# Performance work log

Measured on AMD Instinct MI355X. Metric: run time of the kernel, lower is better.

Reference implementation:

```python
import jax, jax.numpy as jnp
import numpy as np

N, E, D_IN, HEADS, C = 100000, 1600000, 128, 4, 32  # C = out_channels per head


def setup_inputs() -> dict:
    key = jax.random.key(0)
    ks = jax.random.split(key, 10)
    s = 1.0 / np.sqrt(D_IN)
    return {
        "x": jax.random.normal(ks[0], (N, D_IN), jnp.float32),
        "edge_index": jax.random.randint(ks[1], (2, E), 0, N, jnp.int64),
        "Wq": jax.random.normal(ks[2], (D_IN, HEADS * C), jnp.float32) * s,
        "bq": jnp.zeros((HEADS * C,), jnp.float32),
        "Wk": jax.random.normal(ks[3], (D_IN, HEADS * C), jnp.float32) * s,
        "bk": jnp.zeros((HEADS * C,), jnp.float32),
        "Wv": jax.random.normal(ks[4], (D_IN, HEADS * C), jnp.float32) * s,
        "bv": jnp.zeros((HEADS * C,), jnp.float32),
        "Wskip": jax.random.normal(ks[5], (D_IN, HEADS * C), jnp.float32) * s,
        "bskip": jnp.zeros((HEADS * C,), jnp.float32),
    }


def reference(x, edge_index, Wq, bq, Wk, bk, Wv, bv, Wskip, bskip):
    n = x.shape[0]
    src, dst = edge_index[0], edge_index[1]  # message flows src (j) -> dst (i)
    q = (x @ Wq + bq).reshape(n, HEADS, C)
    k = (x @ Wk + bk).reshape(n, HEADS, C)
    v = (x @ Wv + bv).reshape(n, HEADS, C)

    # per-edge attention logits [E, H]
    alpha = jnp.einsum('ehc,ehc->eh', q[dst], k[src]) / jnp.sqrt(jnp.float32(C))

    # segment softmax over incoming edges of each target node
    m = jax.ops.segment_max(alpha, dst, num_segments=n)          # [N, H]
    p = jnp.exp(alpha - m[dst])                                   # [E, H]
    z = jax.ops.segment_sum(p, dst, num_segments=n)               # [N, H]
    w = p / (z[dst] + 1e-16)                                      # [E, H]

    # softmax-weighted scatter aggregation of values
    out = jax.ops.segment_sum(v[src] * w[:, :, None], dst, num_segments=n)
    out = out.reshape(n, HEADS * C)

    # root/skip connection (beta=False default: plain add)
    out = out + x @ Wskip + bskip
    return out
```

## Files before the change

### kernel.cpp

```cpp
#include <hip/hip_runtime.h>

#define DIN 128
#define NHEADS 4
#define CH 32
#define MT 64
#define NPB 256
#define EPB_IT 25
#define BCAP 6144

#define ST_H 136

typedef _Float16 h8 __attribute__((ext_vector_type(8)));
typedef _Float16 h2 __attribute__((ext_vector_type(2)));
typedef float f4 __attribute__((ext_vector_type(4)));

__global__ __launch_bounds__(256) void prep_w(
    const float* __restrict__ Wq, const float* __restrict__ Wk,
    const float* __restrict__ Wv, const float* __restrict__ Wsk,
    _Float16* __restrict__ wt)
{
    int i = blockIdx.x * 256 + threadIdx.x;
    if (i >= 4 * 16384) return;
    int mat = i >> 14;
    int rem = i & 16383;
    int n  = rem >> 7;
    int kk = rem & 127;
    const float* W = (mat == 0) ? Wq : (mat == 1) ? Wk : (mat == 2) ? Wv : Wsk;
    wt[i] = (_Float16)W[kk * 128 + n];
}

__global__ __launch_bounds__(256) void qkvs_mat(
    const float* __restrict__ x, const _Float16* __restrict__ wt,
    const float* __restrict__ bq, const float* __restrict__ bk,
    const float* __restrict__ bv, const float* __restrict__ bsk,
    _Float16* __restrict__ qh, _Float16* __restrict__ kh,
    _Float16* __restrict__ vh, _Float16* __restrict__ skiph, int N)
{
    __shared__ _Float16 Sbuf[MT * ST_H];
    const int t = threadIdx.x;
    const int mat = blockIdx.x;
    const int rowBase = blockIdx.y * MT;

    for (int i = t; i < MT * 16; i += 256) {
        int r  = i >> 4;
        int c8 = i & 15;
        int gr = rowBase + r;
        _Float16 h[8];
        if (gr < N) {
            float4 f0 = reinterpret_cast<const float4*>(x)[(size_t)gr * 32 + c8 * 2];
            float4 f1 = reinterpret_cast<const float4*>(x)[(size_t)gr * 32 + c8 * 2 + 1];
            h[0] = (_Float16)f0.x; h[1] = (_Float16)f0.y;
            h[2] = (_Float16)f0.z; h[3] = (_Float16)f0.w;
            h[4] = (_Float16)f1.x; h[5] = (_Float16)f1.y;
            h[6] = (_Float16)f1.z; h[7] = (_Float16)f1.w;
        } else {
            #pragma unroll
            for (int j = 0; j < 8; ++j) h[j] = (_Float16)0.f;
        }
        *reinterpret_cast<uint4*>(&Sbuf[r * 128 + ((c8 ^ (r & 7)) << 3)]) =
            *reinterpret_cast<uint4*>(h);
    }
    __syncthreads();

    const int wid  = t >> 6;
    const int l    = t & 63;
    const int lm   = l & 15;
    const int quad = l >> 4;

    const _Float16* __restrict__ Bsrc = wt + (size_t)mat * 16384;

    f4 acc[8];
    #pragma unroll
    for (int nt = 0; nt < 8; ++nt)
        acc[nt] = (f4){0.f, 0.f, 0.f, 0.f};

    #pragma unroll
    for (int kq = 0; kq < 4; ++kq) {
        const int c8 = kq * 4 + quad;
        const int k0 = c8 << 3;
        h8 a0 = *reinterpret_cast<const h8*>(
            &Sbuf[(wid * 16 + lm) * 128 + ((c8 ^ (lm & 7)) << 3)]);
        #pragma unroll
        for (int nt = 0; nt < 8; ++nt) {
            h8 b = *reinterpret_cast<const h8*>(
                &Bsrc[(size_t)(nt * 16 + lm) * 128 + k0]);
            acc[nt] = __builtin_amdgcn_mfma_f32_16x16x32_f16(a0, b, acc[nt], 0, 0, 0);
        }
    }
    __syncthreads();

    const float* bias = (mat == 0) ? bq : (mat == 1) ? bk : (mat == 2) ? bv : bsk;

    #pragma unroll
    for (int nt = 0; nt < 8; ++nt) {
        int col = nt * 16 + lm;
        float bsv = bias[col];
        int row = wid * 16 + quad * 4;
        #pragma unroll
        for (int i2 = 0; i2 < 4; ++i2)
            Sbuf[(row + i2) * ST_H + col] = (_Float16)(acc[nt][i2] + bsv);
    }
    __syncthreads();

    _Float16* __restrict__ dst = (mat == 0) ? qh : (mat == 1) ? kh
                               : (mat == 2) ? vh : skiph;
    for (int j = t; j < MT * 16; j += 256) {
        int r  = j >> 4;
        int c0 = (j & 15) << 3;
        int gr = rowBase + r;
        if (gr < N)
            *reinterpret_cast<uint4*>(&dst[(size_t)gr * 128 + c0]) =
                *reinterpret_cast<const uint4*>(&Sbuf[r * ST_H + c0]);
    }
}

__global__ __launch_bounds__(256) void bucket_scatter(
    const int* __restrict__ ei, int* __restrict__ bcur,
    unsigned* __restrict__ pairs, int E, int nb)
{
    __shared__ int cnt[512];
    int t = threadIdx.x;
    for (int b = t; b < nb; b += 256) cnt[b] = 0;
    __syncthreads();

    long long e0 = (long long)blockIdx.x * (256 * EPB_IT);
    int ps[EPB_IT], pd[EPB_IT];
    #pragma unroll
    for (int j = 0; j < EPB_IT; ++j) {
        long long e = e0 + j * 256 + t;
        if (e < E) {
            ps[j] = ei[e];
            pd[j] = ei[(size_t)E + e];
            atomicAdd(&cnt[pd[j] >> 8], 1);
        } else pd[j] = -1;
    }
    __syncthreads();
    for (int b = t; b < nb; b += 256) {
        int c = cnt[b];
        if (c) cnt[b] = b * BCAP + atomicAdd(&bcur[b], c);
    }
    __syncthreads();
    #pragma unroll
    for (int j = 0; j < EPB_IT; ++j) {
        if (pd[j] >= 0) {
            int pos = atomicAdd(&cnt[pd[j] >> 8], 1);
            pairs[pos] = ((unsigned)ps[j] << 8) | ((unsigned)pd[j] & 255u);
        }
    }
}

__global__ __launch_bounds__(512) void scan_buckets(
    const int* __restrict__ bcur, int* __restrict__ boff, int nb)
{
    __shared__ int ws[8];
    int t = threadIdx.x, lane = t & 63, wid = t >> 6;
    int v = (t < nb) ? bcur[t] : 0;
    int s = v;
    #pragma unroll
    for (int off = 1; off < 64; off <<= 1) {
        int n = __shfl_up(s, off);
        if (lane >= off) s += n;
    }
    if (lane == 63) ws[wid] = s;
    __syncthreads();
    int add = 0;
    for (int w = 0; w < wid; ++w) add += ws[w];
    int excl = s - v + add;
    if (t < nb) boff[t] = excl;
    if (t == nb - 1) boff[nb] = excl + v;
}

__global__ __launch_bounds__(256) void bucket_finalize(
    const unsigned* __restrict__ pairs, const int* __restrict__ bcur,
    const int* __restrict__ boff,
    int* __restrict__ rowptr, int* __restrict__ sorted, int N, int nb)
{
    __shared__ int cnt[NPB];
    __shared__ int cur[NPB];
    __shared__ int ws[4];
    __shared__ int sbuf[BCAP];
    int b = blockIdx.x, t = threadIdx.x;
    cnt[t] = 0;
    __syncthreads();
    size_t r0 = (size_t)b * BCAP;
    int sz = bcur[b];
    int w0 = boff[b];
    for (int i = t; i < sz; i += 256)
        atomicAdd(&cnt[pairs[r0 + i] & (NPB - 1)], 1);
    __syncthreads();

    int v = cnt[t];
    int lane = t & 63, wid = t >> 6;
    int incl = v;
    #pragma unroll
    for (int off = 1; off < 64; off <<= 1) {
        int n = __shfl_up(incl, off);
        if (lane >= off) incl += n;
    }
    if (lane == 63) ws[wid] = incl;
    __syncthreads();
    int add = 0;
    for (int w = 0; w < wid; ++w) add += ws[w];
    int lbase = (incl - v) + add;

    int node = b * NPB + t;
    if (node < N) rowptr[node] = w0 + lbase;
    if (b == nb - 1 && t == 0) rowptr[N] = boff[nb];
    cur[t] = lbase;
    __syncthreads();

    for (int i = t; i < sz; i += 256) {
        unsigned pr = pairs[r0 + i];
        int lpos = atomicAdd(&cur[pr & (NPB - 1)], 1);
        sbuf[lpos] = (int)(pr >> 8);
    }
    __syncthreads();
    for (int i = t; i < sz; i += 256)
        sorted[w0 + i] = sbuf[i];
}

__device__ inline float4 cvt4(unsigned lo, unsigned hi) {
    union { unsigned u[2]; _Float16 h[4]; } c;
    c.u[0] = lo; c.u[1] = hi;
    return make_float4((float)c.h[0], (float)c.h[1], (float)c.h[2], (float)c.h[3]);
}

__device__ inline h2 as_h2(unsigned u) {
    union { unsigned u; h2 h; } c;
    c.u = u;
    return c.h;
}

__global__ __launch_bounds__(256) void node_aggregate(
    const _Float16* __restrict__ q, const _Float16* __restrict__ kh,
    const _Float16* __restrict__ vh, const _Float16* __restrict__ skiph,
    const int* __restrict__ rowptr, const int* __restrict__ srcs,
    float* __restrict__ out, int N)
{
    int gid  = blockIdx.x * 256 + threadIdx.x;
    int node = gid >> 5;
    if (node >= N) return;
    int l = gid & 31;

    uint2 qu = reinterpret_cast<const uint2*>(q + (size_t)node * 128)[l];
    h2 qa = as_h2(qu.x), qb = as_h2(qu.y);

    float4 acc = make_float4(0.f, 0.f, 0.f, 0.f);
    float z = 0.f;

    const uint2* k2 = reinterpret_cast<const uint2*>(kh);
    const uint2* v2 = reinterpret_cast<const uint2*>(vh);
    const float SC = 0.17677669529663687f;
    int e0 = rowptr[node], e1 = rowptr[node + 1];
    int e = e0;

    for (; e + 8 <= e1; e += 8) {
        int s[8];
        #pragma unroll
        for (int j = 0; j < 8; ++j) s[j] = srcs[e + j];
        uint2 kr[8], vr[8];
        #pragma unroll
        for (int j = 0; j < 8; ++j) kr[j] = k2[(size_t)s[j] * 32 + l];
        #pragma unroll
        for (int j = 0; j < 8; ++j) vr[j] = v2[(size_t)s[j] * 32 + l];

        float sv[8];
        #pragma unroll
        for (int j = 0; j < 8; ++j) {
            sv[j] = __builtin_amdgcn_fdot2(qa, as_h2(kr[j].x),
                    __builtin_amdgcn_fdot2(qb, as_h2(kr[j].y), 0.f, false), false);
        }
        #pragma unroll
        for (int j = 0; j < 8; ++j) sv[j] += __shfl_xor(sv[j], 1);
        #pragma unroll
        for (int j = 0; j < 8; ++j) sv[j] += __shfl_xor(sv[j], 2);
        #pragma unroll
        for (int j = 0; j < 8; ++j) sv[j] += __shfl_xor(sv[j], 4);

        #pragma unroll
        for (int j = 0; j < 8; ++j) {
            float p = __expf(sv[j] * SC);
            float4 v = cvt4(vr[j].x, vr[j].y);
            z += p;
            acc.x += p * v.x; acc.y += p * v.y;
            acc.z += p * v.z; acc.w += p * v.w;
        }
    }
    for (; e < e1; ++e) {
        int s0 = srcs[e];
        uint2 kr = k2[(size_t)s0 * 32 + l];
        uint2 vr = v2[(size_t)s0 * 32 + l];
        float sa = __builtin_amdgcn_fdot2(qa, as_h2(kr.x),
                   __builtin_amdgcn_fdot2(qb, as_h2(kr.y), 0.f, false), false);
        sa += __shfl_xor(sa, 1);
        sa += __shfl_xor(sa, 2);
        sa += __shfl_xor(sa, 4);
        float pa = __expf(sa * SC);
        float4 v0 = cvt4(vr.x, vr.y);
        z += pa;
        acc.x += pa * v0.x; acc.y += pa * v0.y;
        acc.z += pa * v0.z; acc.w += pa * v0.w;
    }

    uint2 su = reinterpret_cast<const uint2*>(skiph + (size_t)node * 128)[l];
    float4 sk = cvt4(su.x, su.y);
    float inv = 1.f / (z + 1e-16f);
    float4 o;
    o.x = sk.x + acc.x * inv; o.y = sk.y + acc.y * inv;
    o.z = sk.z + acc.z * inv; o.w = sk.w + acc.w * inv;
    reinterpret_cast<float4*>(out)[(size_t)node * 32 + l] = o;
}

extern "C" void kernel_launch(void* const* d_in, const int* in_sizes, int n_in,
                              void* d_out, int out_size, void* d_ws, size_t ws_size,
                              hipStream_t stream)
{
    const float* x   = (const float*)d_in[0];
    const int*   ei  = (const int*)d_in[1];
    const float* Wq  = (const float*)d_in[2];
    const float* bq  = (const float*)d_in[3];
    const float* Wk  = (const float*)d_in[4];
    const float* bk  = (const float*)d_in[5];
    const float* Wv  = (const float*)d_in[6];
    const float* bv  = (const float*)d_in[7];
    const float* Wsk = (const float*)d_in[8];
    const float* bsk = (const float*)d_in[9];
    float* out = (float*)d_out;

    const int N = in_sizes[0] / DIN;
    const int E = in_sizes[1] / 2;
    const int nb = (N + NPB - 1) / NPB;

    _Float16* qh    = (_Float16*)d_ws;
    _Float16* kh    = qh + (size_t)N * DIN;
    _Float16* vh    = kh + (size_t)N * DIN;
    _Float16* skiph = vh + (size_t)N * DIN;
    _Float16* wt    = skiph + (size_t)N * DIN;
    unsigned* pairs = (unsigned*)(wt + 4 * 16384);
    int* sorted   = (int*)(pairs + (size_t)nb * BCAP);
    int* rowptr   = sorted + E;
    int* bcur     = rowptr + (N + 1);
    int* boff     = bcur + 512;

    hipMemsetAsync(bcur, 0, 512 * sizeof(int), stream);

    prep_w<<<(4 * 16384 + 255) / 256, 256, 0, stream>>>(Wq, Wk, Wv, Wsk, wt);

    dim3 ggrid(4, (N + MT - 1) / MT);
    qkvs_mat<<<ggrid, 256, 0, stream>>>(x, wt, bq, bk, bv, bsk,
                                        qh, kh, vh, skiph, N);

    int sb = (E + 256 * EPB_IT - 1) / (256 * EPB_IT);
    bucket_scatter<<<sb, 256, 0, stream>>>(ei, bcur, pairs, E, nb);
    scan_buckets<<<1, 512, 0, stream>>>(bcur, boff, nb);
    bucket_finalize<<<nb, 256, 0, stream>>>(pairs, bcur, boff, rowptr, sorted, N, nb);

    int ab = (N * 32 + 255) / 256;
    node_aggregate<<<ab, 256, 0, stream>>>(qh, kh, vh, skiph, rowptr, sorted, out, N);
}
```

Before: 389.0 us.

## Interleave K and V per node and compute projection pairs per block

The projection kernel now computes two weight matrices per block (Q+skip, or K+V) and reuses the loaded x tile, halving the number of x reads. K and V are written into one interleaved buffer so that each lane's 4 K halves and 4 V halves sit next to each other. The aggregation kernel can then fetch both with a single 16-byte load per edge instead of two separate 8-byte gathers. This cuts the number of gather transactions in the edge loop, at the cost of more shared memory and registers in the projection kernel.

New measurement: 381.1 us. -2.0%, faster.

```diff
diff --git a/kernel.cpp b/kernel.cpp
--- a/kernel.cpp
+++ b/kernel.cpp
@@ -9,6 +9,7 @@
 #define BCAP 6144
 
 #define ST_H 136
+#define ST_KV 264
 
 typedef _Float16 h8 __attribute__((ext_vector_type(8)));
 typedef _Float16 h2 __attribute__((ext_vector_type(2)));
@@ -29,16 +30,16 @@
     wt[i] = (_Float16)W[kk * 128 + n];
 }
 
-__global__ __launch_bounds__(256) void qkvs_mat(
+__global__ __launch_bounds__(256) void qkvs_pair(
     const float* __restrict__ x, const _Float16* __restrict__ wt,
     const float* __restrict__ bq, const float* __restrict__ bk,
     const float* __restrict__ bv, const float* __restrict__ bsk,
-    _Float16* __restrict__ qh, _Float16* __restrict__ kh,
-    _Float16* __restrict__ vh, _Float16* __restrict__ skiph, int N)
-{
-    __shared__ _Float16 Sbuf[MT * ST_H];
+    _Float16* __restrict__ qh, _Float16* __restrict__ kvh,
+    _Float16* __restrict__ skiph, int N)
+{
+    __shared__ _Float16 Sbuf[17408];
     const int t = threadIdx.x;
-    const int mat = blockIdx.x;
+    const int pair = blockIdx.x;
     const int rowBase = blockIdx.y * MT;
 
     for (int i = t; i < MT * 16; i += 256) {
@@ -67,50 +68,87 @@
     const int lm   = l & 15;
     const int quad = l >> 4;
 
-    const _Float16* __restrict__ Bsrc = wt + (size_t)mat * 16384;
-
-    f4 acc[8];
-    #pragma unroll
-    for (int nt = 0; nt < 8; ++nt)
-        acc[nt] = (f4){0.f, 0.f, 0.f, 0.f};
-
+    h8 afrag[4];
     #pragma unroll
     for (int kq = 0; kq < 4; ++kq) {
-        const int c8 = kq * 4 + quad;
-        const int k0 = c8 << 3;
-        h8 a0 = *reinterpret_cast<const h8*>(
+        int c8 = kq * 4 + quad;
+        afrag[kq] = *reinterpret_cast<const h8*>(
             &Sbuf[(wid * 16 + lm) * 128 + ((c8 ^ (lm & 7)) << 3)]);
-        #pragma unroll
-        for (int nt = 0; nt < 8; ++nt) {
-            h8 b = *reinterpret_cast<const h8*>(
-                &Bsrc[(size_t)(nt * 16 + lm) * 128 + k0]);
-            acc[nt] = __builtin_amdgcn_mfma_f32_16x16x32_f16(a0, b, acc[nt], 0, 0, 0);
-        }
-    }
-    __syncthreads();
-
-    const float* bias = (mat == 0) ? bq : (mat == 1) ? bk : (mat == 2) ? bv : bsk;
-
-    #pragma unroll
-    for (int nt = 0; nt < 8; ++nt) {
-        int col = nt * 16 + lm;
-        float bsv = bias[col];
-        int row = wid * 16 + quad * 4;
-        #pragma unroll
-        for (int i2 = 0; i2 < 4; ++i2)
-            Sbuf[(row + i2) * ST_H + col] = (_Float16)(acc[nt][i2] + bsv);
-    }
-    __syncthreads();
-
-    _Float16* __restrict__ dst = (mat == 0) ? qh : (mat == 1) ? kh
-                               : (mat == 2) ? vh : skiph;
-    for (int j = t; j < MT * 16; j += 256) {
-        int r  = j >> 4;
-        int c0 = (j & 15) << 3;
-        int gr = rowBase + r;
-        if (gr < N)
-            *reinterpret_cast<uint4*>(&dst[(size_t)gr * 128 + c0]) =
-                *reinterpret_cast<const uint4*>(&Sbuf[r * ST_H + c0]);
+    }
+    __syncthreads();
+
+    #pragma unroll
+    for (int half = 0; half < 2; ++half) {
+        const int mat = (pair == 0) ? (half == 0 ? 0 : 3)
+                                    : (half == 0 ? 1 : 2);
+        const _Float16* __restrict__ Bsrc = wt + (size_t)mat * 16384;
+
+        f4 acc[8];
+        #pragma unroll
+        for (int nt = 0; nt < 8; ++nt)
+            acc[nt] = (f4){0.f, 0.f, 0.f, 0.f};
+
+        #pragma unroll
+        for (int kq = 0; kq < 4; ++kq) {
+            const int k0 = (kq * 4 + quad) << 3;
+            #pragma unroll
+            for (int nt = 0; nt < 8; ++nt) {
+                h8 b = *reinterpret_cast<const h8*>(
+                    &Bsrc[(size_t)(nt * 16 + lm) * 128 + k0]);
+                acc[nt] = __builtin_amdgcn_mfma_f32_16x16x32_f16(afrag[kq], b, acc[nt], 0, 0, 0);
+            }
+        }
+
+        const float* bias = (mat == 0) ? bq : (mat == 1) ? bk : (mat == 2) ? bv : bsk;
+
+        if (pair == 0) {
+            _Float16* St = Sbuf + half * (MT * ST_H);
+            #pragma unroll
+            for (int nt = 0; nt < 8; ++nt) {
+                int col = nt * 16 + lm;
+                float bsv = bias[col];
+                int row = wid * 16 + quad * 4;
+                #pragma unroll
+                for (int i2 = 0; i2 < 4; ++i2)
+                    St[(row + i2) * ST_H + col] = (_Float16)(acc[nt][i2] + bsv);
+            }
+        } else {
+            const int off = half * 4;
+            #pragma unroll
+            for (int nt = 0; nt < 8; ++nt) {
+                int col = nt * 16 + lm;
+                float bsv = bias[col];
+                int row = wid * 16 + quad * 4;
+                int sc = ((col >> 2) << 3) + (col & 3) + off;
+                #pragma unroll
+                for (int i2 = 0; i2 < 4; ++i2)
+                    Sbuf[(row + i2) * ST_KV + sc] = (_Float16)(acc[nt][i2] + bsv);
+            }
+        }
+    }
+    __syncthreads();
+
+    if (pair == 0) {
+        for (int j = t; j < 2048; j += 256) {
+            int half = j >> 10;
+            int jj = j & 1023;
+            int r  = jj >> 4;
+            int c0 = (jj & 15) << 3;
+            int gr = rowBase + r;
+            _Float16* __restrict__ dst = half ? skiph : qh;
+            if (gr < N)
+                *reinterpret_cast<uint4*>(&dst[(size_t)gr * 128 + c0]) =
+                    *reinterpret_cast<const uint4*>(&Sbuf[half * (MT * ST_H) + r * ST_H + c0]);
+        }
+    } else {
+        for (int j = t; j < 2048; j += 256) {
+            int r = j >> 5;
+            int g = j & 31;
+            int gr = rowBase + r;
+            if (gr < N)
+                *reinterpret_cast<uint4*>(&kvh[(size_t)gr * 256 + g * 8]) =
+                    *reinterpret_cast<const uint4*>(&Sbuf[r * ST_KV + g * 8]);
+        }
     }
 }
 
@@ -232,8 +270,8 @@
 }
 
 __global__ __launch_bounds__(256) void node_aggregate(
-    const _Float16* __restrict__ q, const _Float16* __restrict__ kh,
-    const _Float16* __restrict__ vh, const _Float16* __restrict__ skiph,
+    const _Float16* __restrict__ q, const _Float16* __restrict__ kv,
+    const _Float16* __restrict__ skiph,
     const int* __restrict__ rowptr, const int* __restrict__ srcs,
     float* __restrict__ out, int N)
 {
@@ -248,8 +286,7 @@
     float4 acc = make_float4(0.f, 0.f, 0.f, 0.f);
     float z = 0.f;
 
-    const uint2* k2 = reinterpret_cast<const uint2*>(kh);
-    const uint2* v2 = reinterpret_cast<const uint2*>(vh);
+    const uint4* kv4 = reinterpret_cast<const uint4*>(kv);
     const float SC = 0.17677669529663687f;
     int e0 = rowptr[node], e1 = rowptr[node + 1];
     int e = e0;
@@ -258,17 +295,15 @@
         int s[8];
         #pragma unroll
         for (int j = 0; j < 8; ++j) s[j] = srcs[e + j];
-        uint2 kr[8], vr[8];
-        #pragma unroll
-        for (int j = 0; j < 8; ++j) kr[j] = k2[(size_t)s[j] * 32 + l];
-        #pragma unroll
-        for (int j = 0; j < 8; ++j) vr[j] = v2[(size_t)s[j] * 32 + l];
+        uint4 r[8];
+        #pragma unroll
+        for (int j = 0; j < 8; ++j) r[j] = kv4[(size_t)s[j] * 32 + l];
 
         float sv[8];
         #pragma unroll
         for (int j = 0; j < 8; ++j) {
-            sv[j] = __builtin_amdgcn_fdot2(qa, as_h2(kr[j].x),
-                    __builtin_amdgcn_fdot2(qb, as_h2(kr[j].y), 0.f, false), false);
+            sv[j] = __builtin_amdgcn_fdot2(qa, as_h2(r[j].x),
+                    __builtin_amdgcn_fdot2(qb, as_h2(r[j].y), 0.f, false), false);
         }
         #pragma unroll
         for (int j = 0; j < 8; ++j) sv[j] += __shfl_xor(sv[j], 1);
@@ -280,7 +315,7 @@
         #pragma unroll
         for (int j = 0; j < 8; ++j) {
             float p = __expf(sv[j] * SC);
-            float4 v = cvt4(vr[j].x, vr[j].y);
+            float4 v = cvt4(r[j].z, r[j].w);
             z += p;
             acc.x += p * v.x; acc.y += p * v.y;
             acc.z += p * v.z; acc.w += p * v.w;
@@ -288,15 +323,14 @@
     }
     for (; e < e1; ++e) {
         int s0 = srcs[e];
-        uint2 kr = k2[(size_t)s0 * 32 + l];
-        uint2 vr = v2[(size_t)s0 * 32 + l];
-        float sa = __builtin_amdgcn_fdot2(qa, as_h2(kr.x),
-                   __builtin_amdgcn_fdot2(qb, as_h2(kr.y), 0.f, false), false);
+        uint4 r0 = kv4[(size_t)s0 * 32 + l];
+        float sa = __builtin_amdgcn_fdot2(qa, as_h2(r0.x),
+                   __builtin_amdgcn_fdot2(qb, as_h2(r0.y), 0.f, false), false);
         sa += __shfl_xor(sa, 1);
         sa += __shfl_xor(sa, 2);
         sa += __shfl_xor(sa, 4);
         float pa = __expf(sa * SC);
-        float4 v0 = cvt4(vr.x, vr.y);
+        float4 v0 = cvt4(r0.z, r0.w);
         z += pa;
         acc.x += pa * v0.x; acc.y += pa * v0.y;
         acc.z += pa * v0.z; acc.w += pa * v0.w;
@@ -332,9 +366,8 @@
     const int nb = (N + NPB - 1) / NPB;
 
     _Float16* qh    = (_Float16*)d_ws;
-    _Float16* kh    = qh + (size_t)N * DIN;
-    _Float16* vh    = kh + (size_t)N * DIN;
-    _Float16* skiph = vh + (size_t)N * DIN;
+    _Float16* kvh   = qh + (size_t)N * DIN;
+    _Float16* skiph = kvh + (size_t)N * 256;
     _Float16* wt    = skiph + (size_t)N * DIN;
     unsigned* pairs = (unsigned*)(wt + 4 * 16384);
     int* sorted   = (int*)(pairs + (size_t)nb * BCAP);
@@ -346,9 +379,9 @@
 
     prep_w<<<(4 * 16384 + 255) / 256, 256, 0, stream>>>(Wq, Wk, Wv, Wsk, wt);
 
-    dim3 ggrid(4, (N + MT - 1) / MT);
-    qkvs_mat<<<ggrid, 256, 0, stream>>>(x, wt, bq, bk, bv, bsk,
-                                        qh, kh, vh, skiph, N);
+    dim3 ggrid(2, (N + MT - 1) / MT);
+    qkvs_pair<<<ggrid, 256, 0, stream>>>(x, wt, bq, bk, bv, bsk,
+                                         qh, kvh, skiph, N);
 
     int sb = (E + 256 * EPB_IT - 1) / (256 * EPB_IT);
     bucket_scatter<<<sb, 256, 0, stream>>>(ei, bcur, pairs, E, nb);
@@ -356,5 +389,5 @@
     bucket_finalize<<<nb, 256, 0, stream>>>(pairs, bcur, boff, rowptr, sorted, N, nb);
 
     int ab = (N * 32 + 255) / 256;
-    node_aggregate<<<ab, 256, 0, stream>>>(qh, kh, vh, skiph, rowptr, sorted, out, N);
-}
+    node_aggregate<<<ab, 256, 0, stream>>>(qh, kvh, skiph, rowptr, sorted, out, N);
+}
```
